# Kernel optimization log

Hardware: AMD Instinct MI355X
Metric: run time of the kernel (lower is better)

Reference implementation:

```python
import jax, jax.numpy as jnp
import numpy as np

B, T, OBS = 4096, 256, 64
NHID, LAT = 128, 32

def setup_inputs() -> dict:
    key = jax.random.key(0)
    ks = jax.random.split(key, 5)
    return {
        "data": jax.random.normal(ks[0], (B, T, OBS), dtype=jnp.float32),
        "W_i2h": jax.random.normal(ks[1], (NHID, OBS + NHID), dtype=jnp.float32) * 0.05,
        "b_i2h": jax.random.normal(ks[2], (NHID,), dtype=jnp.float32) * 0.05,
        "W_h2o": jax.random.normal(ks[3], (LAT, NHID), dtype=jnp.float32) * 0.05,
        "b_h2o": jax.random.normal(ks[4], (LAT,), dtype=jnp.float32) * 0.05,
        "time_dim": T,
    }

def reference(data, W_i2h, b_i2h, W_h2o, b_h2o, time_dim):
    # data: [B, T, obs_dim]; RNN scan over time (encoder=False branch).
    batch = data.shape[0]
    nhidden = W_i2h.shape[0]
    h0 = jnp.zeros((batch, nhidden), dtype=data.dtype)

    def step(h, x_t):
        # combined = cat(x, h) -> tanh(i2h) -> h2o
        combined = jnp.concatenate([x_t, h], axis=1)       # [B, obs+nhid]
        h_new = jnp.tanh(combined @ W_i2h.T + b_i2h)       # [B, nhid]
        out_t = h_new @ W_h2o.T + b_h2o                    # [B, latent]
        return h_new, out_t

    _, outs = jax.lax.scan(step, h0, jnp.swapaxes(data, 0, 1))  # [T, B, latent]
    return jnp.swapaxes(outs, 0, 1)                             # [B, T, latent]
```

## Files before the change

### kernel.cpp

```cpp
#include <hip/hip_runtime.h>
#include <hip/hip_bf16.h>

typedef float f32x4 __attribute__((ext_vector_type(4)));
typedef short s16x8 __attribute__((ext_vector_type(8)));
typedef short s16x4 __attribute__((ext_vector_type(4)));

#define NHID 128
#define OBS  64
#define LAT  32
#define KTOT 192
#define BB   16
#define LDB  328

static __device__ __forceinline__ unsigned short f2bf(float x) {
    __hip_bfloat16 h = __float2bfloat16(x);
    return *reinterpret_cast<unsigned short*>(&h);
}

static __device__ __forceinline__ float fast_tanh(float x) {
    float ax = __builtin_fabsf(x);
    float e  = __expf(-2.0f * ax);
    float r  = __fdividef(1.0f - e, 1.0f + e);
    return __builtin_copysignf(r, x);
}

__global__ __launch_bounds__(256) void rnn_fused(
    const float* __restrict__ data,
    const float* __restrict__ W1,
    const float* __restrict__ b1,
    const float* __restrict__ Wo,
    const float* __restrict__ bo,
    float* __restrict__ out,
    int T)
{
    __shared__ __align__(16) unsigned short comb[BB * LDB];

    const int tid  = threadIdx.x;
    const int wid  = tid >> 6;
    const int lane = tid & 63;
    const int lr   = lane & 15;
    const int lg   = lane >> 4;
    const int b0   = blockIdx.x * BB;

    const int j0 = wid * 32;
    s16x8 w1f[2][6];
    float bi[2][4];
    for (int jt = 0; jt < 2; ++jt) {
        const float* wrow = W1 + (size_t)(j0 + jt * 16 + lr) * KTOT + lg * 8;
        for (int kf = 0; kf < 6; ++kf) {
            float4 a = *reinterpret_cast<const float4*>(wrow + kf * 32);
            float4 c = *reinterpret_cast<const float4*>(wrow + kf * 32 + 4);
            s16x8 f;
            f[0]=f2bf(a.x); f[1]=f2bf(a.y); f[2]=f2bf(a.z); f[3]=f2bf(a.w);
            f[4]=f2bf(c.x); f[5]=f2bf(c.y); f[6]=f2bf(c.z); f[7]=f2bf(c.w);
            w1f[jt][kf] = f;
        }
        for (int r = 0; r < 4; ++r)
            bi[jt][r] = b1[j0 + jt * 16 + lg * 4 + r];
    }

    s16x8 wof[2][4];
    float bof[2][4];
    if (wid == 0) {
        for (int lt = 0; lt < 2; ++lt) {
            const float* wrow = Wo + (size_t)(lt * 16 + lr) * NHID + lg * 8;
            for (int kt = 0; kt < 4; ++kt) {
                float4 a = *reinterpret_cast<const float4*>(wrow + kt * 32);
                float4 c = *reinterpret_cast<const float4*>(wrow + kt * 32 + 4);
                s16x8 f;
                f[0]=f2bf(a.x); f[1]=f2bf(a.y); f[2]=f2bf(a.z); f[3]=f2bf(a.w);
                f[4]=f2bf(c.x); f[5]=f2bf(c.y); f[6]=f2bf(c.z); f[7]=f2bf(c.w);
                wof[lt][kt] = f;
            }
            for (int r = 0; r < 4; ++r)
                bof[lt][r] = bo[lt * 16 + lg * 4 + r];
        }
    }

    {
        int idx = tid * 8;
        int b   = idx >> 7;
        int jj  = idx & 127;
        *reinterpret_cast<uint4*>(&comb[b * LDB + 64 + jj]) = make_uint4(0,0,0,0);
    }
    const int xb = tid >> 4;
    const int xk = (tid & 15) * 4;
    {
        float4 x = *reinterpret_cast<const float4*>(
            data + ((size_t)(b0 + xb) * T + 0) * OBS + xk);
        s16x4 px;
        px[0]=f2bf(x.x); px[1]=f2bf(x.y); px[2]=f2bf(x.z); px[3]=f2bf(x.w);
        *reinterpret_cast<s16x4*>(&comb[xb * LDB + xk]) = px;
    }
    __syncthreads();

    float4 xpA = *reinterpret_cast<const float4*>(
        data + ((size_t)(b0 + xb) * T + (T > 1 ? 1 : 0)) * OBS + xk);

    int p = 0;
    for (int t = 0; t < T; ++t) {
        int tn = (t + 2 < T) ? t + 2 : T - 1;
        float4 xpB = *reinterpret_cast<const float4*>(
            data + ((size_t)(b0 + xb) * T + tn) * OBS + xk);

        const unsigned short* crow = comb + lr * LDB;
        s16x8 bfr[6];
        bfr[0] = *reinterpret_cast<const s16x8*>(crow + lg * 8);
        bfr[1] = *reinterpret_cast<const s16x8*>(crow + 32 + lg * 8);
        const int hoff = 64 + p * 128;
        for (int kf = 0; kf < 4; ++kf)
            bfr[2 + kf] = *reinterpret_cast<const s16x8*>(crow + hoff + kf * 32 + lg * 8);

        f32x4 acc[2];
        for (int jt = 0; jt < 2; ++jt) {
            f32x4 a;
            a[0]=bi[jt][0]; a[1]=bi[jt][1]; a[2]=bi[jt][2]; a[3]=bi[jt][3];
            for (int kf = 0; kf < 6; ++kf)
                a = __builtin_amdgcn_mfma_f32_16x16x32_bf16(w1f[jt][kf], bfr[kf], a, 0, 0, 0);
            acc[jt] = a;
        }

        const int hw_off = 64 + (1 - p) * 128;
        for (int jt = 0; jt < 2; ++jt) {
            s16x4 hw;
            for (int r = 0; r < 4; ++r)
                hw[r] = f2bf(fast_tanh(acc[jt][r]));
            *reinterpret_cast<s16x4*>(
                &comb[lr * LDB + hw_off + j0 + jt * 16 + lg * 4]) = hw;
        }
        __syncthreads();

        if (wid == 0) {
            s16x8 hf[4];
            const unsigned short* hrow = comb + lr * LDB + hw_off;
            for (int kt = 0; kt < 4; ++kt)
                hf[kt] = *reinterpret_cast<const s16x8*>(hrow + kt * 32 + lg * 8);
            for (int lt = 0; lt < 2; ++lt) {
                f32x4 o;
                o[0]=bof[lt][0]; o[1]=bof[lt][1]; o[2]=bof[lt][2]; o[3]=bof[lt][3];
                for (int kt = 0; kt < 4; ++kt)
                    o = __builtin_amdgcn_mfma_f32_16x16x32_bf16(wof[lt][kt], hf[kt], o, 0, 0, 0);
                float4 st;
                st.x=o[0]; st.y=o[1]; st.z=o[2]; st.w=o[3];
                *reinterpret_cast<float4*>(
                    out + ((size_t)(b0 + lr) * T + t) * LAT + lt * 16 + lg * 4) = st;
            }
        }

        {
            s16x4 px;
            px[0]=f2bf(xpA.x); px[1]=f2bf(xpA.y); px[2]=f2bf(xpA.z); px[3]=f2bf(xpA.w);
            *reinterpret_cast<s16x4*>(&comb[xb * LDB + xk]) = px;
        }
        xpA = xpB;
        __syncthreads();
        p ^= 1;
    }
}

extern "C" void kernel_launch(void* const* d_in, const int* in_sizes, int n_in,
                              void* d_out, int out_size, void* d_ws, size_t ws_size,
                              hipStream_t stream) {
    const float* data = (const float*)d_in[0];
    const float* W1   = (const float*)d_in[1];
    const float* b1   = (const float*)d_in[2];
    const float* Wo   = (const float*)d_in[3];
    const float* bo   = (const float*)d_in[4];
    float* out = (float*)d_out;

    const int B = 4096;
    const int T = in_sizes[0] / (B * OBS);

    dim3 grid(B / BB);
    rnn_fused<<<grid, 256, 0, stream>>>(data, W1, b1, Wo, bo, out, T);
}
```

Measured before the change: 542.1 us.

## Run each batch tile in a single wavefront to remove block barriers

Each 16-row batch tile now runs in one 64-lane wavefront instead of four waves. That wave holds all W_i2h fragments (8x6 bf16 MFMA operands) and the output weights in registers, so the two __syncthreads per timestep go away and only a small LDS round trip is needed to transpose h. The input prefetch is double-buffered in registers and the loop is unrolled by two. tanh now uses exp2 and rcp intrinsics. The trade-off is heavier register pressure and fewer waves per CU (256 single-wave blocks), which may reduce latency hiding, in exchange for removing cross-wave barrier stalls on the serial time dependence.

```diff
diff --git a/kernel.cpp b/kernel.cpp
--- a/kernel.cpp
+++ b/kernel.cpp
@@ -3,28 +3,34 @@
 
 typedef float f32x4 __attribute__((ext_vector_type(4)));
 typedef short s16x8 __attribute__((ext_vector_type(8)));
-typedef short s16x4 __attribute__((ext_vector_type(4)));
 
-#define NHID 128
-#define OBS  64
-#define LAT  32
-#define KTOT 192
-#define BB   16
-#define LDB  328
+#define OBS   64
+#define NHID  128
+#define LAT   32
+#define KTOT  192
+#define BB    16
+#define HSTR  68
 
 static __device__ __forceinline__ unsigned short f2bf(float x) {
     __hip_bfloat16 h = __float2bfloat16(x);
     return *reinterpret_cast<unsigned short*>(&h);
 }
-
+static __device__ __forceinline__ unsigned int pack2(float a, float b) {
+    return ((unsigned int)f2bf(b) << 16) | (unsigned int)f2bf(a);
+}
 static __device__ __forceinline__ float fast_tanh(float x) {
-    float ax = __builtin_fabsf(x);
-    float e  = __expf(-2.0f * ax);
-    float r  = __fdividef(1.0f - e, 1.0f + e);
-    return __builtin_copysignf(r, x);
+    float e = __builtin_amdgcn_exp2f(x * 2.8853900817779268f);
+    float r = __builtin_amdgcn_rcpf(e + 1.0f);
+    return __builtin_fmaf(-2.0f, r, 1.0f);
+}
+static __device__ __forceinline__ s16x8 pack8(float4 a, float4 b) {
+    s16x8 f;
+    f[0]=(short)f2bf(a.x); f[1]=(short)f2bf(a.y); f[2]=(short)f2bf(a.z); f[3]=(short)f2bf(a.w);
+    f[4]=(short)f2bf(b.x); f[5]=(short)f2bf(b.y); f[6]=(short)f2bf(b.z); f[7]=(short)f2bf(b.w);
+    return f;
 }
 
-__global__ __launch_bounds__(256) void rnn_fused(
+__global__ __launch_bounds__(64, 1) void rnn_wave(
     const float* __restrict__ data,
     const float* __restrict__ W1,
     const float* __restrict__ b1,
@@ -33,129 +39,115 @@
     float* __restrict__ out,
     int T)
 {
-    __shared__ __align__(16) unsigned short comb[BB * LDB];
+    __shared__ __align__(16) unsigned int hbuf[BB * HSTR];
 
-    const int tid  = threadIdx.x;
-    const int wid  = tid >> 6;
-    const int lane = tid & 63;
-    const int lr   = lane & 15;
-    const int lg   = lane >> 4;
-    const int b0   = blockIdx.x * BB;
+    const int l  = threadIdx.x;
+    const int b  = l & 15;
+    const int lg = l >> 4;
+    const int b0 = blockIdx.x * BB;
 
-    const int j0 = wid * 32;
-    s16x8 w1f[2][6];
-    float bi[2][4];
-    for (int jt = 0; jt < 2; ++jt) {
-        const float* wrow = W1 + (size_t)(j0 + jt * 16 + lr) * KTOT + lg * 8;
+    s16x8 w1f[8][6];
+    f32x4 b1f[8];
+    #pragma unroll
+    for (int jt = 0; jt < 8; ++jt) {
+        const float* wrow = W1 + (size_t)(jt * 16 + b) * KTOT + lg * 8;
+        #pragma unroll
         for (int kf = 0; kf < 6; ++kf) {
             float4 a = *reinterpret_cast<const float4*>(wrow + kf * 32);
             float4 c = *reinterpret_cast<const float4*>(wrow + kf * 32 + 4);
-            s16x8 f;
-            f[0]=f2bf(a.x); f[1]=f2bf(a.y); f[2]=f2bf(a.z); f[3]=f2bf(a.w);
-            f[4]=f2bf(c.x); f[5]=f2bf(c.y); f[6]=f2bf(c.z); f[7]=f2bf(c.w);
-            w1f[jt][kf] = f;
+            w1f[jt][kf] = pack8(a, c);
         }
-        for (int r = 0; r < 4; ++r)
-            bi[jt][r] = b1[j0 + jt * 16 + lg * 4 + r];
+        b1f[jt] = *reinterpret_cast<const f32x4*>(b1 + jt * 16 + lg * 4);
+    }
+    s16x8 wof[2][4];
+    f32x4 bof_[2];
+    #pragma unroll
+    for (int lt = 0; lt < 2; ++lt) {
+        const float* wrow = Wo + (size_t)(lt * 16 + b) * NHID + lg * 8;
+        #pragma unroll
+        for (int kt = 0; kt < 4; ++kt) {
+            float4 a = *reinterpret_cast<const float4*>(wrow + kt * 32);
+            float4 c = *reinterpret_cast<const float4*>(wrow + kt * 32 + 4);
+            wof[lt][kt] = pack8(a, c);
+        }
+        bof_[lt] = *reinterpret_cast<const f32x4*>(bo + lt * 16 + lg * 4);
     }
 
-    s16x8 wof[2][4];
-    float bof[2][4];
-    if (wid == 0) {
-        for (int lt = 0; lt < 2; ++lt) {
-            const float* wrow = Wo + (size_t)(lt * 16 + lr) * NHID + lg * 8;
-            for (int kt = 0; kt < 4; ++kt) {
-                float4 a = *reinterpret_cast<const float4*>(wrow + kt * 32);
-                float4 c = *reinterpret_cast<const float4*>(wrow + kt * 32 + 4);
-                s16x8 f;
-                f[0]=f2bf(a.x); f[1]=f2bf(a.y); f[2]=f2bf(a.z); f[3]=f2bf(a.w);
-                f[4]=f2bf(c.x); f[5]=f2bf(c.y); f[6]=f2bf(c.z); f[7]=f2bf(c.w);
-                wof[lt][kt] = f;
-            }
-            for (int r = 0; r < 4; ++r)
-                bof[lt][r] = bo[lt * 16 + lg * 4 + r];
-        }
+    const float* xrp  = data + (size_t)(b0 + b) * T * OBS + lg * 8;
+    float*       orow = out  + (size_t)(b0 + b) * T * LAT + lg * 4;
+
+    s16x8 hfr[4];
+    #pragma unroll
+    for (int kf = 0; kf < 4; ++kf)
+        #pragma unroll
+        for (int i = 0; i < 8; ++i) hfr[kf][i] = 0;
+
+    float4 pA[4], pB[4];
+    s16x8  xA[2], xB[2];
+    {
+        pA[0] = *reinterpret_cast<const float4*>(xrp);
+        pA[1] = *reinterpret_cast<const float4*>(xrp + 4);
+        pA[2] = *reinterpret_cast<const float4*>(xrp + 32);
+        pA[3] = *reinterpret_cast<const float4*>(xrp + 36);
+        xA[0] = pack8(pA[0], pA[1]);
+        xA[1] = pack8(pA[2], pA[3]);
+        const float* q = xrp + (size_t)(T > 1 ? 1 : 0) * OBS;
+        pB[0] = *reinterpret_cast<const float4*>(q);
+        pB[1] = *reinterpret_cast<const float4*>(q + 4);
+        pB[2] = *reinterpret_cast<const float4*>(q + 32);
+        pB[3] = *reinterpret_cast<const float4*>(q + 36);
     }
 
-    {
-        int idx = tid * 8;
-        int b   = idx >> 7;
-        int jj  = idx & 127;
-        *reinterpret_cast<uint4*>(&comb[b * LDB + 64 + jj]) = make_uint4(0,0,0,0);
-    }
-    const int xb = tid >> 4;
-    const int xk = (tid & 15) * 4;
-    {
-        float4 x = *reinterpret_cast<const float4*>(
-            data + ((size_t)(b0 + xb) * T + 0) * OBS + xk);
-        s16x4 px;
-        px[0]=f2bf(x.x); px[1]=f2bf(x.y); px[2]=f2bf(x.z); px[3]=f2bf(x.w);
-        *reinterpret_cast<s16x4*>(&comb[xb * LDB + xk]) = px;
-    }
-    __syncthreads();
-
-    float4 xpA = *reinterpret_cast<const float4*>(
-        data + ((size_t)(b0 + xb) * T + (T > 1 ? 1 : 0)) * OBS + xk);
-
-    int p = 0;
-    for (int t = 0; t < T; ++t) {
-        int tn = (t + 2 < T) ? t + 2 : T - 1;
-        float4 xpB = *reinterpret_cast<const float4*>(
-            data + ((size_t)(b0 + xb) * T + tn) * OBS + xk);
-
-        const unsigned short* crow = comb + lr * LDB;
-        s16x8 bfr[6];
-        bfr[0] = *reinterpret_cast<const s16x8*>(crow + lg * 8);
-        bfr[1] = *reinterpret_cast<const s16x8*>(crow + 32 + lg * 8);
-        const int hoff = 64 + p * 128;
-        for (int kf = 0; kf < 4; ++kf)
-            bfr[2 + kf] = *reinterpret_cast<const s16x8*>(crow + hoff + kf * 32 + lg * 8);
-
-        f32x4 acc[2];
-        for (int jt = 0; jt < 2; ++jt) {
-            f32x4 a;
-            a[0]=bi[jt][0]; a[1]=bi[jt][1]; a[2]=bi[jt][2]; a[3]=bi[jt][3];
-            for (int kf = 0; kf < 6; ++kf)
-                a = __builtin_amdgcn_mfma_f32_16x16x32_bf16(w1f[jt][kf], bfr[kf], a, 0, 0, 0);
+    auto body = [&](int t, s16x8 (&xc)[2], float4 (&pn)[4], float4 (&pnn)[4],
+                    s16x8 (&xn)[2]) {
+        {
+            int tn = (t + 2 < T) ? t + 2 : T - 1;
+            const float* q = xrp + (size_t)tn * OBS;
+            pnn[0] = *reinterpret_cast<const float4*>(q);
+            pnn[1] = *reinterpret_cast<const float4*>(q + 4);
+            pnn[2] = *reinterpret_cast<const float4*>(q + 32);
+            pnn[3] = *reinterpret_cast<const float4*>(q + 36);
+        }
+        f32x4 acc[8];
+        #pragma unroll
+        for (int jt = 0; jt < 8; ++jt) {
+            f32x4 a = b1f[jt];
+            a = __builtin_amdgcn_mfma_f32_16x16x32_bf16(w1f[jt][0], xc[0], a, 0, 0, 0);
+            a = __builtin_amdgcn_mfma_f32_16x16x32_bf16(w1f[jt][1], xc[1], a, 0, 0, 0);
+            a = __builtin_amdgcn_mfma_f32_16x16x32_bf16(w1f[jt][2], hfr[0], a, 0, 0, 0);
+            a = __builtin_amdgcn_mfma_f32_16x16x32_bf16(w1f[jt][3], hfr[1], a, 0, 0, 0);
+            a = __builtin_amdgcn_mfma_f32_16x16x32_bf16(w1f[jt][4], hfr[2], a, 0, 0, 0);
+            a = __builtin_amdgcn_mfma_f32_16x16x32_bf16(w1f[jt][5], hfr[3], a, 0, 0, 0);
             acc[jt] = a;
         }
+        #pragma unroll
+        for (int jt = 0; jt < 8; ++jt) {
+            unsigned int w0 = pack2(fast_tanh(acc[jt][0]), fast_tanh(acc[jt][1]));
+            unsigned int w1 = pack2(fast_tanh(acc[jt][2]), fast_tanh(acc[jt][3]));
+            *reinterpret_cast<uint2*>(&hbuf[b * HSTR + jt * 8 + lg * 2]) =
+                make_uint2(w0, w1);
+        }
+        #pragma unroll
+        for (int kf = 0; kf < 4; ++kf)
+            hfr[kf] = *reinterpret_cast<const s16x8*>(&hbuf[b * HSTR + kf * 16 + lg * 4]);
+        #pragma unroll
+        for (int lt = 0; lt < 2; ++lt) {
+            f32x4 o = bof_[lt];
+            #pragma unroll
+            for (int kt = 0; kt < 4; ++kt)
+                o = __builtin_amdgcn_mfma_f32_16x16x32_bf16(wof[lt][kt], hfr[kt], o, 0, 0, 0);
+            *reinterpret_cast<f32x4*>(orow + (size_t)t * LAT + lt * 16) = o;
+        }
+        xn[0] = pack8(pn[0], pn[1]);
+        xn[1] = pack8(pn[2], pn[3]);
+    };
 
-        const int hw_off = 64 + (1 - p) * 128;
-        for (int jt = 0; jt < 2; ++jt) {
-            s16x4 hw;
-            for (int r = 0; r < 4; ++r)
-                hw[r] = f2bf(fast_tanh(acc[jt][r]));
-            *reinterpret_cast<s16x4*>(
-                &comb[lr * LDB + hw_off + j0 + jt * 16 + lg * 4]) = hw;
-        }
-        __syncthreads();
-
-        if (wid == 0) {
-            s16x8 hf[4];
-            const unsigned short* hrow = comb + lr * LDB + hw_off;
-            for (int kt = 0; kt < 4; ++kt)
-                hf[kt] = *reinterpret_cast<const s16x8*>(hrow + kt * 32 + lg * 8);
-            for (int lt = 0; lt < 2; ++lt) {
-                f32x4 o;
-                o[0]=bof[lt][0]; o[1]=bof[lt][1]; o[2]=bof[lt][2]; o[3]=bof[lt][3];
-                for (int kt = 0; kt < 4; ++kt)
-                    o = __builtin_amdgcn_mfma_f32_16x16x32_bf16(wof[lt][kt], hf[kt], o, 0, 0, 0);
-                float4 st;
-                st.x=o[0]; st.y=o[1]; st.z=o[2]; st.w=o[3];
-                *reinterpret_cast<float4*>(
-                    out + ((size_t)(b0 + lr) * T + t) * LAT + lt * 16 + lg * 4) = st;
-            }
-        }
-
-        {
-            s16x4 px;
-            px[0]=f2bf(xpA.x); px[1]=f2bf(xpA.y); px[2]=f2bf(xpA.z); px[3]=f2bf(xpA.w);
-            *reinterpret_cast<s16x4*>(&comb[xb * LDB + xk]) = px;
-        }
-        xpA = xpB;
-        __syncthreads();
-        p ^= 1;
+    for (int t = 0; t + 1 < T; t += 2) {
+        body(t,     xA, pB, pA, xB);
+        body(t + 1, xB, pA, pB, xA);
     }
+    if (T & 1)
+        body(T - 1, xA, pB, pA, xB);
 }
 
 extern "C" void kernel_launch(void* const* d_in, const int* in_sizes, int n_in,
@@ -172,5 +164,5 @@
     const int T = in_sizes[0] / (B * OBS);
 
     dim3 grid(B / BB);
-    rnn_fused<<<grid, 256, 0, stream>>>(data, W1, b1, Wo, bo, out, T);
+    rnn_wave<<<grid, 64, 0, stream>>>(data, W1, b1, Wo, bo, out, T);
 }
```

Result: slower. 754.9 us (+39.3%).
